# Kernel tuning notes

Measured on AMD Instinct MI355X. Metric: run time of the kernel, lower is better.

Reference implementation:

```python
import jax, jax.numpy as jnp
import numpy as np

B, S, D = 1, 2048, 4096
H, KVH, DH = 32, 8, 128          # nheads, kv heads, head dim (GQA expansion = 4)
HID = 11008                       # 256 * ceil(4096 * (8/3) / 256)
EPS = 1e-5
ROPE_BASE = 10000.0


def setup_inputs() -> dict:
    key = jax.random.key(0)
    ks = jax.random.split(key, 10)
    std = 0.02
    w = lambda k, shape: jax.random.normal(k, shape, dtype=jnp.float32) * std
    return {
        "x": jax.random.normal(ks[0], (B, S, D), dtype=jnp.float32),
        "position_ids": jnp.broadcast_to(jnp.arange(S, dtype=jnp.int32), (B, S)),
        "ln_w": jnp.ones((D,), dtype=jnp.float32),
        "ffln_w": jnp.ones((D,), dtype=jnp.float32),
        "wq": w(ks[1], (D, H * DH)),
        "wk": w(ks[2], (D, KVH * DH)),
        "wv": w(ks[3], (D, KVH * DH)),
        "wo": w(ks[4], (H * DH, D)),
        "wg": w(ks[5], (D, HID)),
        "w1": w(ks[6], (D, HID)),
        "w2": w(ks[7], (HID, D)),
    }


def rmsnorm(x, w, eps=EPS):
    # LayerNormParameterized(use_mean=False, use_high_precision_pow=True)
    xf = x.astype(jnp.float32)
    var = jnp.mean(xf * xf, axis=-1, keepdims=True)
    return (xf * jax.lax.rsqrt(var + eps)).astype(x.dtype) * w


def rope(x, pos):
    # interleaved (complex-pair) rotary embedding; x: [B,S,h,DH], pos: [B,S]
    dh = x.shape[-1]
    inv_freq = 1.0 / (ROPE_BASE ** (jnp.arange(0, dh, 2, dtype=jnp.float32) / dh))
    ang = pos.astype(jnp.float32)[:, :, None, None] * inv_freq  # [B,S,1,dh/2]
    cos, sin = jnp.cos(ang), jnp.sin(ang)
    x1, x2 = x[..., 0::2], x[..., 1::2]
    return jnp.stack([x1 * cos - x2 * sin, x1 * sin + x2 * cos], axis=-1).reshape(x.shape)


def block(x, position_ids, ln_w, ffln_w, wq, wk, wv, wo, wg, w1, w2):
    # --- attention sublayer ---
    a = rmsnorm(x, ln_w)
    q = (a @ wq).reshape(B, S, H, DH)
    k = (a @ wk).reshape(B, S, KVH, DH)
    v = (a @ wv).reshape(B, S, KVH, DH)
    q = rope(q, position_ids)
    k = rope(k, position_ids)
    # GQA expansion: kv head g serves query heads [g*exp, (g+1)*exp)
    exp = H // KVH
    k_e = jnp.repeat(k, exp, axis=2)  # [B,S,H,DH]
    v_e = jnp.repeat(v, exp, axis=2)
    scores = jnp.einsum("bqhd,bkhd->bhqk", q, k_e) / np.sqrt(DH).astype(np.float32)
    causal = jnp.tril(jnp.ones((S, S), dtype=bool))
    scores = jnp.where(causal, scores, jnp.finfo(scores.dtype).min)
    p = jax.nn.softmax(scores, axis=-1)
    attn = jnp.einsum("bhqk,bkhd->bqhd", p, v_e).reshape(B, S, H * DH)
    x = x + attn @ wo
    # --- SwiGLU FFN sublayer ---
    b = rmsnorm(x, ffln_w)
    ff = (jax.nn.silu(b @ wg) * (b @ w1)) @ w2
    return x + ff


def reference(x, position_ids, ln_w, ffln_w, wq, wk, wv, wo, wg, w1, w2):
    return block(x, position_ids, ln_w, ffln_w, wq, wk, wv, wo, wg, w1, w2)
```

## Files before the change

kernel.cpp:

```cpp
#include <hip/hip_runtime.h>
#include <hip/hip_bf16.h>

typedef __bf16 bf16_t;
typedef __bf16 bf16x4 __attribute__((ext_vector_type(4)));
typedef __bf16 bf16x8 __attribute__((ext_vector_type(8)));
typedef float f32x4 __attribute__((ext_vector_type(4)));

#define S_ 2048
#define D_ 4096
#define H_ 32
#define KVH_ 8
#define DH_ 128
#define HID_ 11008
#define QKV_N 6144
#define GU_N 22016

__device__ __forceinline__ void gl16(const bf16_t* g, bf16_t* l) {
  __builtin_amdgcn_global_load_lds(
      (const __attribute__((address_space(1))) unsigned int*)g,
      (__attribute__((address_space(3))) unsigned int*)l, 16, 0, 0);
}

#define VMW(N)                                          \
  asm volatile("s_waitcnt vmcnt(" #N ")" ::: "memory"); \
  __builtin_amdgcn_sched_barrier(0)

#define LGKM(N)                                           \
  asm volatile("s_waitcnt lgkmcnt(" #N ")" ::: "memory"); \
  __builtin_amdgcn_sched_barrier(0)

#define BAR()                          \
  asm volatile("" ::: "memory");       \
  __builtin_amdgcn_s_barrier();        \
  asm volatile("" ::: "memory")

__global__ __launch_bounds__(256) void rmsnorm_kernel(
    const float* __restrict__ x, const float* __restrict__ w,
    bf16_t* __restrict__ out) {
  int row = blockIdx.x;
  const float* xr = x + (size_t)row * D_;
  float ss = 0.f;
  #pragma unroll
  for (int it = 0; it < 4; ++it) {
    int i = threadIdx.x * 4 + it * 1024;
    float4 v = *(const float4*)(xr + i);
    ss += v.x * v.x + v.y * v.y + v.z * v.z + v.w * v.w;
  }
  #pragma unroll
  for (int off = 32; off; off >>= 1) ss += __shfl_xor(ss, off);
  __shared__ float s4[4];
  if ((threadIdx.x & 63) == 0) s4[threadIdx.x >> 6] = ss;
  __syncthreads();
  float tot = s4[0] + s4[1] + s4[2] + s4[3];
  float rinv = rsqrtf(tot / (float)D_ + 1e-5f);
  bf16_t* orow = out + (size_t)row * D_;
  #pragma unroll
  for (int it = 0; it < 4; ++it) {
    int i = threadIdx.x * 4 + it * 1024;
    float4 v = *(const float4*)(xr + i);
    orow[i + 0] = (bf16_t)(v.x * rinv * w[i + 0]);
    orow[i + 1] = (bf16_t)(v.y * rinv * w[i + 1]);
    orow[i + 2] = (bf16_t)(v.z * rinv * w[i + 2]);
    orow[i + 3] = (bf16_t)(v.w * rinv * w[i + 3]);
  }
}

__global__ __launch_bounds__(256) void combine_rms_kernel(
    const float* __restrict__ x, const float* __restrict__ p0,
    const float* __restrict__ p1, const float* __restrict__ w,
    float* __restrict__ x1, bf16_t* __restrict__ out) {
  int row = blockIdx.x;
  size_t base = (size_t)row * D_;
  float ss = 0.f;
  float4 vals[4];
  #pragma unroll
  for (int it = 0; it < 4; ++it) {
    int i = threadIdx.x * 4 + it * 1024;
    float4 a = *(const float4*)(x + base + i);
    float4 b = *(const float4*)(p0 + base + i);
    float4 c = *(const float4*)(p1 + base + i);
    float4 v;
    v.x = a.x + b.x + c.x; v.y = a.y + b.y + c.y;
    v.z = a.z + b.z + c.z; v.w = a.w + b.w + c.w;
    vals[it] = v;
    *(float4*)(x1 + base + i) = v;
    ss += v.x * v.x + v.y * v.y + v.z * v.z + v.w * v.w;
  }
  #pragma unroll
  for (int off = 32; off; off >>= 1) ss += __shfl_xor(ss, off);
  __shared__ float s4[4];
  if ((threadIdx.x & 63) == 0) s4[threadIdx.x >> 6] = ss;
  __syncthreads();
  float tot = s4[0] + s4[1] + s4[2] + s4[3];
  float rinv = rsqrtf(tot / (float)D_ + 1e-5f);
  #pragma unroll
  for (int it = 0; it < 4; ++it) {
    int i = threadIdx.x * 4 + it * 1024;
    float4 v = vals[it];
    out[base + i + 0] = (bf16_t)(v.x * rinv * w[i + 0]);
    out[base + i + 1] = (bf16_t)(v.y * rinv * w[i + 1]);
    out[base + i + 2] = (bf16_t)(v.z * rinv * w[i + 2]);
    out[base + i + 3] = (bf16_t)(v.w * rinv * w[i + 3]);
  }
}

__global__ __launch_bounds__(256) void combine_out_kernel(
    const float* __restrict__ x1, const float* __restrict__ p0,
    const float* __restrict__ p1, float* __restrict__ outp) {
  size_t i = ((size_t)blockIdx.x * 256 + threadIdx.x) * 4;
  float4 a = *(const float4*)(x1 + i);
  float4 b = *(const float4*)(p0 + i);
  float4 c = *(const float4*)(p1 + i);
  float4 v;
  v.x = a.x + b.x + c.x; v.y = a.y + b.y + c.y;
  v.z = a.z + b.z + c.z; v.w = a.w + b.w + c.w;
  *(float4*)(outp + i) = v;
}

__global__ __launch_bounds__(256) void wtrans_kernel(
    const float* __restrict__ W, bf16_t* __restrict__ WT, int K, int N) {
  __shared__ bf16_t t[32][258];
  int k0 = blockIdx.x * 32, n0 = blockIdx.y * 256;
  #pragma unroll
  for (int i = 0; i < 8; ++i) {
    int flat = i * 1024 + threadIdx.x * 4;
    int kk = flat >> 8, nn = flat & 255;
    float4 wv = *(const float4*)(W + (size_t)(k0 + kk) * N + n0 + nn);
    bf16_t* p = &t[kk][nn];
    p[0] = (bf16_t)wv.x; p[1] = (bf16_t)wv.y;
    p[2] = (bf16_t)wv.z; p[3] = (bf16_t)wv.w;
  }
  __syncthreads();
  int kc8 = (threadIdx.x & 3) * 8;
  #pragma unroll
  for (int i = 0; i < 4; ++i) {
    int nn = i * 64 + (threadIdx.x >> 2);
    bf16x8 vals;
    #pragma unroll
    for (int j = 0; j < 8; ++j) vals[j] = t[kc8 + j][nn];
    *(bf16x8*)(WT + (size_t)(n0 + nn) * K + k0 + kc8) = vals;
  }
}

__global__ __launch_bounds__(256) void vtrans_kernel(
    const bf16_t* __restrict__ qkv, bf16_t* __restrict__ vt) {
  __shared__ bf16_t t[64][72];
  int s0 = blockIdx.x * 64, d0 = blockIdx.y * 64;
  #pragma unroll
  for (int it = 0; it < 2; ++it) {
    int r = (threadIdx.x >> 3) + it * 32;
    int c = (threadIdx.x & 7) * 8;
    *(bf16x8*)&t[r][c] =
        *(const bf16x8*)(qkv + (size_t)(s0 + r) * QKV_N + 5120 + d0 + c);
  }
  __syncthreads();
  #pragma unroll
  for (int it = 0; it < 2; ++it) {
    int c = threadIdx.x & 63;
    int sb = (threadIdx.x >> 6) * 16 + it * 8;
    bf16x8 v;
    #pragma unroll
    for (int j = 0; j < 8; ++j) v[j] = t[sb + j][c];
    *(bf16x8*)(vt + (size_t)(d0 + c) * S_ + s0 + sb) = v;
  }
}

__global__ __launch_bounds__(256) void rope_table_kernel(
    const int* __restrict__ pos_ids, float* __restrict__ cos_t,
    float* __restrict__ sin_t) {
  int idx = blockIdx.x * 256 + threadIdx.x;
  int s = idx >> 6, i = idx & 63;
  float pos = (float)pos_ids[s];
  float inv_freq = exp2f(-(float)i * (13.287712379549449f / 64.0f));
  float ang = pos * inv_freq;
  cos_t[idx] = cosf(ang);
  sin_t[idx] = sinf(ang);
}

__global__ __launch_bounds__(256) void rope_kernel(
    bf16_t* __restrict__ buf, const float* __restrict__ cos_t,
    const float* __restrict__ sin_t, int nheads, int colbase, int total) {
  int idx = blockIdx.x * 256 + threadIdx.x;
  if (idx >= total) return;
  int i = idx & 63;
  int t2 = idx >> 6;
  int s = t2 / nheads, h = t2 % nheads;
  size_t base = (size_t)s * QKV_N + colbase + h * 128 + 2 * i;
  float x1 = (float)buf[base], x2 = (float)buf[base + 1];
  float c = cos_t[s * 64 + i], sn = sin_t[s * 64 + i];
  buf[base]     = (bf16_t)(x1 * c - x2 * sn);
  buf[base + 1] = (bf16_t)(x1 * sn + x2 * c);
}


#define READ_A(dst, BIx, KK, MH)                                           \
  _Pragma("unroll") for (int m = 0; m < 4; ++m)                            \
    dst[m] = *(const bf16x8*)&lds[BIx][0][wr][KK]                          \
        [((MH) * 64 + m * 16 + fr) * 32 + rc * 8];

#define READ_B(dst, BIx, KK)                                               \
  _Pragma("unroll") for (int n = 0; n < 4; ++n)                            \
    dst[n] = *(const bf16x8*)&lds[BIx][1][wcH][KK]                         \
        [(wcL * 64 + n * 16 + fr) * 32 + rc * 8];

#define MFMA16(aS, bS, MH)                                                 \
  __builtin_amdgcn_s_setprio(1);                                           \
  _Pragma("unroll") for (int m = 0; m < 4; ++m)                            \
    _Pragma("unroll") for (int n = 0; n < 4; ++n)                          \
      acc[(MH) * 4 + m][n] = __builtin_amdgcn_mfma_f32_16x16x32_bf16(      \
          aS[m], bS[n], acc[(MH) * 4 + m][n], 0, 0, 0);                    \
  __builtin_amdgcn_s_setprio(0);

#define DO_TILE(BI, T)                                                     \
  {                                                                        \
    const int Tp1 = (T) + 1 < NT, Tp2 = (T) + 2 < NT;                      \
    if (Tp1) {                                                             \
      stage(BI ^ 1, 0, 0, 1, (T) + 1); stage(BI ^ 1, 1, 0, 1, (T) + 1);    \
      stage(BI ^ 1, 0, 1, 1, (T) + 1); stage(BI ^ 1, 1, 1, 1, (T) + 1);    \
    }                                                                      \
    READ_A(aF, BI, 0, 0); READ_B(bF, BI, 0);                               \
    LGKM(0);                                                               \
    MFMA16(aF, bF, 0);                                                     \
    READ_A(aF, BI, 0, 1);                                                  \
    LGKM(0);                                                               \
    MFMA16(aF, bF, 1);                                                     \
    BAR();                     \
    if (Tp2) {                                                             \
      stage(BI, 0, 0, 0, (T) + 2); stage(BI, 1, 0, 0, (T) + 2);            \
      stage(BI, 0, 1, 0, (T) + 2); stage(BI, 1, 1, 0, (T) + 2);            \
    }                                                                      \
    READ_A(aF, BI, 1, 0); READ_B(bF, BI, 1);                               \
    LGKM(0);                                                               \
    MFMA16(aF, bF, 0);                                                     \
    READ_A(aF, BI, 1, 1);                                                  \
    LGKM(0);                                                               \
    MFMA16(aF, bF, 1);                                                     \
    if (Tp2) { VMW(4); } else if (Tp1) { VMW(0); }                         \
    BAR();        \
  }

template <int MODE, int SPLIT>
__global__ __launch_bounds__(512, 2) void gemm256_kernel(
    const bf16_t* __restrict__ A, int lda, const bf16_t* __restrict__ BT,
    int ldb, void* __restrict__ Cout, int ldc, int K) {
  __shared__ __align__(16) bf16_t lds[2][2][2][2][128 * 32];

  const int tid = threadIdx.x;
  const int lane = tid & 63;
  const int wid = tid >> 6;
  const int wr = wid >> 2;
  const int wc = wid & 3;
  const int wcH = wc >> 1, wcL = wc & 1;
  const int g = lane >> 4, fr = lane & 15;
  const int rc = (g + ((fr >> 1) & 3)) & 3;

  const int nwg = gridDim.x;
  const int orig = blockIdx.x;
  int wg = (orig & 7) * (nwg >> 3) + (orig >> 3);
  int kz = 0;
  if constexpr (SPLIT) {
    const int half = nwg >> 1;
    kz = wg >= half;
    wg -= kz * half;
  }
  const int bx = wg & 7;
  const int by = wg >> 3;
  const size_t row0 = (size_t)bx * 256, col0 = (size_t)by * 256;

  const int srow = tid >> 2;
  const int schunk = ((tid & 3) - ((tid >> 3) & 3)) & 3;

  const size_t lda2 = (size_t)lda * 2, ldb2 = (size_t)ldb * 2;
  const size_t kzoff = (size_t)kz * K * 2;
  const char* aB0 =
      (const char*)A + (row0 + srow) * lda2 + schunk * 16 + kzoff;
  const char* aB1 = aB0 + (size_t)128 * lda2;
  const char* bB0 =
      (const char*)BT + (col0 + srow) * ldb2 + schunk * 16 + kzoff;
  const char* bB1 = bB0 + (size_t)128 * ldb2;

  auto stage = [&](int bi, int ab, int h, int kk, int kt) {
    const char* base = ab ? (h ? bB1 : bB0) : (h ? aB1 : aB0);
    gl16((const bf16_t*)(base + (size_t)kt * 128 + kk * 64),
         &lds[bi][ab][h][kk][tid * 8]);
  };

  f32x4 acc[8][4] = {};
  bf16x8 aF[4], bF[4];
  const int NT = K / 64;

  stage(0, 0, 0, 0, 0); stage(0, 1, 0, 0, 0);
  stage(0, 0, 1, 0, 0); stage(0, 1, 1, 0, 0);
  stage(0, 0, 0, 1, 0); stage(0, 1, 0, 1, 0);
  stage(0, 0, 1, 1, 0); stage(0, 1, 1, 1, 0);
  stage(1, 0, 0, 0, 1); stage(1, 1, 0, 0, 1);
  stage(1, 0, 1, 0, 1); stage(1, 1, 1, 0, 1);
  VMW(4);
  BAR();

  for (int T = 0; T < NT; T += 2) {
    DO_TILE(0, T);
    DO_TILE(1, T + 1);
  }

  float* fOut = (float*)Cout + (size_t)kz * 2048 * ldc;
  #pragma unroll
  for (int mf = 0; mf < 8; ++mf)
    #pragma unroll
    for (int n = 0; n < 4; ++n)
      #pragma unroll
      for (int r = 0; r < 4; ++r) {
        size_t row = row0 + wr * 128 + mf * 16 + g * 4 + r;
        size_t col = col0 + wc * 64 + n * 16 + fr;
        float val = acc[mf][n][r];
        if constexpr (MODE == 0) {
          ((bf16_t*)Cout)[row * ldc + col] = (bf16_t)val;
        } else {
          fOut[row * ldc + col] = val;
        }
      }
}

__global__ __launch_bounds__(256, 2) void attn_kernel(
    const bf16_t* __restrict__ qkv, const bf16_t* __restrict__ vt,
    bf16_t* __restrict__ o) {
  int h = blockIdx.y;
  int qb = (S_ / 64 - 1) - blockIdx.x;
  int kvh = h >> 2;
  int tid = threadIdx.x;
  int wid = tid >> 6, lane = tid & 63;
  int g = lane >> 4, fr = lane & 15;

  __shared__ __align__(16) bf16_t kfl[2][8192];
  __shared__ __align__(16) bf16_t vfl[2][8192];
  __shared__ __align__(16) bf16_t p_lds[4][16][72];

  const int fr_s = (tid >> 2) & 15, g_s = tid & 3;
  const int kcw = (tid >> 6) & 3;
  const int kc2w = (tid >> 6) & 1;
  const int nhi = tid >> 7;
  const bf16_t* kSrc = qkv + (size_t)fr_s * QKV_N + 4096 + kvh * 128 +
                       (kcw * 4 + g_s) * 8;
  const bf16_t* vSrc = vt + ((size_t)kvh * 128 + nhi * 16 + fr_s) * S_ +
                       (kc2w * 4 + g_s) * 8;

  auto stage = [&](int bi, int t) {
    size_t kv0 = (size_t)t * 64;
    #pragma unroll
    for (int i = 0; i < 4; ++i)
      gl16(kSrc + (kv0 + i * 16) * QKV_N, &kfl[bi][(i * 256 + tid) * 8]);
    #pragma unroll
    for (int i = 0; i < 4; ++i)
      gl16(vSrc + (size_t)i * 32 * S_ + kv0, &vfl[bi][(i * 256 + tid) * 8]);
  };

  int q0w = qb * 64 + wid * 16;
  bf16x8 q_frag[4];
  const bf16_t* qptr = qkv + (size_t)(q0w + fr) * QKV_N + h * 128;
  #pragma unroll
  for (int kc = 0; kc < 4; ++kc)
    q_frag[kc] = *(const bf16x8*)(qptr + kc * 32 + g * 8);
  VMW(0);

  stage(0, 0);

  f32x4 o_frag[8] = {};
  float m_run[4], l_run[4];
  #pragma unroll
  for (int r = 0; r < 4; ++r) { m_run[r] = -1e30f; l_run[r] = 0.f; }

  const float sc = 0.08838834764831845f * 1.4426950408889634f;

  for (int t = 0; t <= qb; ++t) {
    int cur = t & 1;
    int kv0 = t * 64;
    if (t < qb) {
      stage(cur ^ 1, t + 1);
      VMW(8);
    } else {
      VMW(0);
    }
    BAR();

    f32x4 sfr[4];
    #pragma unroll
    for (int nf = 0; nf < 4; ++nf) {
      f32x4 acc = {};
      #pragma unroll
      for (int kc = 0; kc < 4; ++kc) {
        bf16x8 kf =
            *(const bf16x8*)&kfl[cur][(nf * 256 + kc * 64 + fr * 4 + g) * 8];
        acc = __builtin_amdgcn_mfma_f32_16x16x32_bf16(q_frag[kc], kf, acc, 0, 0, 0);
      }
      sfr[nf] = acc;
    }

    bool diag = (t == qb);
    float mtile[4];
    #pragma unroll
    for (int r = 0; r < 4; ++r) mtile[r] = -1e30f;
    #pragma unroll
    for (int nf = 0; nf < 4; ++nf)
      #pragma unroll
      for (int r = 0; r < 4; ++r) {
        if (diag) {
          int kvg = kv0 + nf * 16 + fr;
          int qg = q0w + 4 * g + r;
          if (kvg > qg) sfr[nf][r] = -1e30f;
        }
        mtile[r] = fmaxf(mtile[r], sfr[nf][r]);
      }
    #pragma unroll
    for (int r = 0; r < 4; ++r) {
      float mv = mtile[r];
      mv = fmaxf(mv, __shfl_xor(mv, 1));
      mv = fmaxf(mv, __shfl_xor(mv, 2));
      mv = fmaxf(mv, __shfl_xor(mv, 4));
      mv = fmaxf(mv, __shfl_xor(mv, 8));
      mtile[r] = mv;
    }
    float alpha[4];
    #pragma unroll
    for (int r = 0; r < 4; ++r) {
      float m_new = fmaxf(m_run[r], mtile[r]);
      alpha[r] = exp2f((m_run[r] - m_new) * sc);
      m_run[r] = m_new;
    }
    float lsum[4] = {0.f, 0.f, 0.f, 0.f};
    #pragma unroll
    for (int nf = 0; nf < 4; ++nf)
      #pragma unroll
      for (int r = 0; r < 4; ++r) {
        float p = exp2f((sfr[nf][r] - m_run[r]) * sc);
        sfr[nf][r] = p;
        lsum[r] += p;
      }
    #pragma unroll
    for (int r = 0; r < 4; ++r) {
      float lv = lsum[r];
      lv += __shfl_xor(lv, 1);
      lv += __shfl_xor(lv, 2);
      lv += __shfl_xor(lv, 4);
      lv += __shfl_xor(lv, 8);
      l_run[r] = l_run[r] * alpha[r] + lv;
    }
    #pragma unroll
    for (int nfo = 0; nfo < 8; ++nfo)
      #pragma unroll
      for (int r = 0; r < 4; ++r) o_frag[nfo][r] *= alpha[r];

    #pragma unroll
    for (int nf = 0; nf < 4; ++nf)
      #pragma unroll
      for (int r = 0; r < 4; ++r)
        p_lds[wid][4 * g + r][nf * 16 + fr] = (bf16_t)sfr[nf][r];

    #pragma unroll
    for (int kc2 = 0; kc2 < 2; ++kc2) {
      bf16x8 pf = *(const bf16x8*)&p_lds[wid][fr][kc2 * 32 + g * 8];
      #pragma unroll
      for (int nfo = 0; nfo < 8; ++nfo) {
        bf16x8 vf =
            *(const bf16x8*)&vfl[cur][(nfo * 128 + kc2 * 64 + fr * 4 + g) * 8];
        o_frag[nfo] = __builtin_amdgcn_mfma_f32_16x16x32_bf16(pf, vf, o_frag[nfo], 0, 0, 0);
      }
    }
    BAR();
  }

  #pragma unroll
  for (int nfo = 0; nfo < 8; ++nfo)
    #pragma unroll
    for (int r = 0; r < 4; ++r) {
      int qg = q0w + 4 * g + r;
      float val = o_frag[nfo][r] / l_run[r];
      o[(size_t)qg * (H_ * DH_) + h * DH_ + nfo * 16 + fr] = (bf16_t)val;
    }
}

__global__ __launch_bounds__(256) void silu_mul_kernel(bf16_t* __restrict__ gu) {
  size_t idx = (size_t)blockIdx.x * 256 + threadIdx.x;
  int r = (int)(idx / (HID_ / 8));
  int c8 = (int)(idx % (HID_ / 8));
  bf16_t* p = gu + (size_t)r * GU_N + c8 * 8;
  bf16x8 g8 = *(const bf16x8*)p;
  bf16x8 u8 = *(const bf16x8*)(p + HID_);
  bf16x8 h8;
  #pragma unroll
  for (int j = 0; j < 8; ++j) {
    float gv = (float)g8[j];
    float uv = (float)u8[j];
    h8[j] = (bf16_t)(gv / (1.f + __expf(-gv)) * uv);
  }
  *(bf16x8*)p = h8;
}

extern "C" void kernel_launch(void* const* d_in, const int* in_sizes, int n_in,
                              void* d_out, int out_size, void* d_ws,
                              size_t ws_size, hipStream_t stream) {
  const float* x = (const float*)d_in[0];
  const int* pos = (const int*)d_in[1];
  const float* ln_w = (const float*)d_in[2];
  const float* ffln_w = (const float*)d_in[3];
  const float* wq = (const float*)d_in[4];
  const float* wk = (const float*)d_in[5];
  const float* wv = (const float*)d_in[6];
  const float* wo = (const float*)d_in[7];
  const float* wg = (const float*)d_in[8];
  const float* w1 = (const float*)d_in[9];
  const float* w2 = (const float*)d_in[10];

  char* ws = (char*)d_ws;
  size_t off = 0;
  auto alloc = [&](size_t bytes) {
    size_t o = off;
    off = (off + bytes + 255) & ~(size_t)255;
    return o;
  };
  bf16_t* Wbuf = (bf16_t*)(ws + alloc((size_t)GU_N * D_ * 2));
  bf16_t* nbuf = (bf16_t*)(ws + alloc((size_t)S_ * D_ * 2));
  bf16_t* qkv  = (bf16_t*)(ws + alloc((size_t)S_ * QKV_N * 2));
  float*  x1   = (float*)(ws + alloc((size_t)S_ * D_ * 4));
  bf16_t* gu   = (bf16_t*)(ws + alloc((size_t)S_ * GU_N * 2));
  bf16_t* vtb  = (bf16_t*)(ws + alloc((size_t)KVH_ * DH_ * S_ * 2));
  float*  cos_t = (float*)(ws + alloc((size_t)S_ * 64 * 4));
  float*  sin_t = (float*)(ws + alloc((size_t)S_ * 64 * 4));
  float* part = (float*)((char*)Wbuf + ((size_t)96 << 20));

  rmsnorm_kernel<<<S_, 256, 0, stream>>>(x, ln_w, nbuf);
  wtrans_kernel<<<dim3(D_ / 32, D_ / 256), 256, 0, stream>>>(wq, Wbuf, D_, D_);
  wtrans_kernel<<<dim3(D_ / 32, 1024 / 256), 256, 0, stream>>>(
      wk, Wbuf + (size_t)4096 * D_, D_, 1024);
  wtrans_kernel<<<dim3(D_ / 32, 1024 / 256), 256, 0, stream>>>(
      wv, Wbuf + (size_t)5120 * D_, D_, 1024);
  rope_table_kernel<<<(S_ * 64) / 256, 256, 0, stream>>>(pos, cos_t, sin_t);
  gemm256_kernel<0, 0><<<dim3((S_ / 256) * (QKV_N / 256)), 512, 0, stream>>>(
      nbuf, D_, Wbuf, D_, qkv, QKV_N, D_);
  rope_kernel<<<(S_ * H_ * 64) / 256, 256, 0, stream>>>(
      qkv, cos_t, sin_t, H_, 0, S_ * H_ * 64);
  rope_kernel<<<(S_ * KVH_ * 64) / 256, 256, 0, stream>>>(
      qkv, cos_t, sin_t, KVH_, 4096, S_ * KVH_ * 64);
  vtrans_kernel<<<dim3(S_ / 64, (KVH_ * DH_) / 64), 256, 0, stream>>>(qkv, vtb);
  attn_kernel<<<dim3(S_ / 64, H_), 256, 0, stream>>>(qkv, vtb, nbuf);
  wtrans_kernel<<<dim3(D_ / 32, D_ / 256), 256, 0, stream>>>(wo, Wbuf, D_, D_);
  gemm256_kernel<2, 1><<<dim3((S_ / 256) * (D_ / 256) * 2), 512, 0, stream>>>(
      nbuf, D_, Wbuf, D_, part, D_, 2048);
  combine_rms_kernel<<<S_, 256, 0, stream>>>(
      x, part, part + (size_t)S_ * D_, ffln_w, x1, nbuf);
  wtrans_kernel<<<dim3(D_ / 32, HID_ / 256), 256, 0, stream>>>(wg, Wbuf, D_, HID_);
  wtrans_kernel<<<dim3(D_ / 32, HID_ / 256), 256, 0, stream>>>(
      w1, Wbuf + (size_t)HID_ * D_, D_, HID_);
  gemm256_kernel<0, 0><<<dim3((S_ / 256) * (GU_N / 256)), 512, 0, stream>>>(
      nbuf, D_, Wbuf, D_, gu, GU_N, D_);
  silu_mul_kernel<<<(S_ * HID_ / 8) / 256, 256, 0, stream>>>(gu);
  wtrans_kernel<<<dim3(HID_ / 32, D_ / 256), 256, 0, stream>>>(w2, Wbuf, HID_, D_);
  gemm256_kernel<2, 1><<<dim3((S_ / 256) * (D_ / 256) * 2), 512, 0, stream>>>(
      gu, GU_N, Wbuf, HID_, part, D_, 5504);
  combine_out_kernel<<<(S_ * D_ / 4) / 256, 256, 0, stream>>>(
      x1, part, part + (size_t)S_ * D_, (float*)d_out);
}
```

Before: 1.204 ms.

## Use 1024-thread GEMM blocks with 64x64 per-wave tiles and simpler pipeline

The 256x256 GEMM goes from 8 waves to 16 waves per block. Each wave now owns a 64x64 output subtile instead of 128x64, which halves the accumulator registers. The deeper split-k-half prefetch schedule is replaced by a single-stage double buffer that waits for all loads (vmcnt 0) every K-tile. The aim is more waves in flight and lower register pressure, at the cost of more LDS reads per MFMA and less overlap between loads and compute. Launch bounds of (1024,4) may force heavy register limits or spills.

```diff
diff --git a/kernel.cpp b/kernel.cpp
--- a/kernel.cpp
+++ b/kernel.cpp
@@ -193,64 +193,35 @@
 }
 
 
-#define READ_A(dst, BIx, KK, MH)                                           \
+#define READ_A(dst, BIx, KK)                                               \
   _Pragma("unroll") for (int m = 0; m < 4; ++m)                            \
-    dst[m] = *(const bf16x8*)&lds[BIx][0][wr][KK]                          \
-        [((MH) * 64 + m * 16 + fr) * 32 + rc * 8];
+    dst[m] = *(const bf16x8*)&lds[BIx][0][KK]                              \
+        [(wr * 64 + m * 16 + fr) * 32 + rc * 8];
 
 #define READ_B(dst, BIx, KK)                                               \
   _Pragma("unroll") for (int n = 0; n < 4; ++n)                            \
-    dst[n] = *(const bf16x8*)&lds[BIx][1][wcH][KK]                         \
-        [(wcL * 64 + n * 16 + fr) * 32 + rc * 8];
-
-#define MFMA16(aS, bS, MH)                                                 \
+    dst[n] = *(const bf16x8*)&lds[BIx][1][KK]                              \
+        [(wc * 64 + n * 16 + fr) * 32 + rc * 8];
+
+#define MFMA16(aS, bS)                                                     \
   __builtin_amdgcn_s_setprio(1);                                           \
   _Pragma("unroll") for (int m = 0; m < 4; ++m)                            \
     _Pragma("unroll") for (int n = 0; n < 4; ++n)                          \
-      acc[(MH) * 4 + m][n] = __builtin_amdgcn_mfma_f32_16x16x32_bf16(      \
-          aS[m], bS[n], acc[(MH) * 4 + m][n], 0, 0, 0);                    \
+      acc[m][n] = __builtin_amdgcn_mfma_f32_16x16x32_bf16(                 \
+          aS[m], bS[n], acc[m][n], 0, 0, 0);                               \
   __builtin_amdgcn_s_setprio(0);
 
-#define DO_TILE(BI, T)                                                     \
-  {                                                                        \
-    const int Tp1 = (T) + 1 < NT, Tp2 = (T) + 2 < NT;                      \
-    if (Tp1) {                                                             \
-      stage(BI ^ 1, 0, 0, 1, (T) + 1); stage(BI ^ 1, 1, 0, 1, (T) + 1);    \
-      stage(BI ^ 1, 0, 1, 1, (T) + 1); stage(BI ^ 1, 1, 1, 1, (T) + 1);    \
-    }                                                                      \
-    READ_A(aF, BI, 0, 0); READ_B(bF, BI, 0);                               \
-    LGKM(0);                                                               \
-    MFMA16(aF, bF, 0);                                                     \
-    READ_A(aF, BI, 0, 1);                                                  \
-    LGKM(0);                                                               \
-    MFMA16(aF, bF, 1);                                                     \
-    BAR();                     \
-    if (Tp2) {                                                             \
-      stage(BI, 0, 0, 0, (T) + 2); stage(BI, 1, 0, 0, (T) + 2);            \
-      stage(BI, 0, 1, 0, (T) + 2); stage(BI, 1, 1, 0, (T) + 2);            \
-    }                                                                      \
-    READ_A(aF, BI, 1, 0); READ_B(bF, BI, 1);                               \
-    LGKM(0);                                                               \
-    MFMA16(aF, bF, 0);                                                     \
-    READ_A(aF, BI, 1, 1);                                                  \
-    LGKM(0);                                                               \
-    MFMA16(aF, bF, 1);                                                     \
-    if (Tp2) { VMW(4); } else if (Tp1) { VMW(0); }                         \
-    BAR();        \
-  }
-
 template <int MODE, int SPLIT>
-__global__ __launch_bounds__(512, 2) void gemm256_kernel(
+__global__ __launch_bounds__(1024, 4) void gemm256_kernel(
     const bf16_t* __restrict__ A, int lda, const bf16_t* __restrict__ BT,
     int ldb, void* __restrict__ Cout, int ldc, int K) {
-  __shared__ __align__(16) bf16_t lds[2][2][2][2][128 * 32];
+  __shared__ __align__(16) bf16_t lds[2][2][2][256 * 32];
 
   const int tid = threadIdx.x;
   const int lane = tid & 63;
   const int wid = tid >> 6;
   const int wr = wid >> 2;
   const int wc = wid & 3;
-  const int wcH = wc >> 1, wcL = wc & 1;
   const int g = lane >> 4, fr = lane & 15;
   const int rc = (g + ((fr >> 1) & 3)) & 3;
 
@@ -272,47 +243,53 @@
 
   const size_t lda2 = (size_t)lda * 2, ldb2 = (size_t)ldb * 2;
   const size_t kzoff = (size_t)kz * K * 2;
-  const char* aB0 =
+  const char* aB =
       (const char*)A + (row0 + srow) * lda2 + schunk * 16 + kzoff;
-  const char* aB1 = aB0 + (size_t)128 * lda2;
-  const char* bB0 =
+  const char* bB =
       (const char*)BT + (col0 + srow) * ldb2 + schunk * 16 + kzoff;
-  const char* bB1 = bB0 + (size_t)128 * ldb2;
-
-  auto stage = [&](int bi, int ab, int h, int kk, int kt) {
-    const char* base = ab ? (h ? bB1 : bB0) : (h ? aB1 : aB0);
+
+  auto stage = [&](int bi, int ab, int kk, int kt) {
+    const char* base = ab ? bB : aB;
     gl16((const bf16_t*)(base + (size_t)kt * 128 + kk * 64),
-         &lds[bi][ab][h][kk][tid * 8]);
+         &lds[bi][ab][kk][tid * 8]);
   };
 
-  f32x4 acc[8][4] = {};
+  f32x4 acc[4][4] = {};
   bf16x8 aF[4], bF[4];
   const int NT = K / 64;
 
-  stage(0, 0, 0, 0, 0); stage(0, 1, 0, 0, 0);
-  stage(0, 0, 1, 0, 0); stage(0, 1, 1, 0, 0);
-  stage(0, 0, 0, 1, 0); stage(0, 1, 0, 1, 0);
-  stage(0, 0, 1, 1, 0); stage(0, 1, 1, 1, 0);
-  stage(1, 0, 0, 0, 1); stage(1, 1, 0, 0, 1);
-  stage(1, 0, 1, 0, 1); stage(1, 1, 1, 0, 1);
-  VMW(4);
+  stage(0, 0, 0, 0); stage(0, 1, 0, 0);
+  stage(0, 0, 1, 0); stage(0, 1, 1, 0);
+  VMW(0);
   BAR();
 
-  for (int T = 0; T < NT; T += 2) {
-    DO_TILE(0, T);
-    DO_TILE(1, T + 1);
+  for (int T = 0; T < NT; ++T) {
+    const int BI = T & 1;
+    const int Tp1 = T + 1 < NT;
+    if (Tp1) {
+      stage(BI ^ 1, 0, 0, T + 1); stage(BI ^ 1, 1, 0, T + 1);
+      stage(BI ^ 1, 0, 1, T + 1); stage(BI ^ 1, 1, 1, T + 1);
+    }
+    READ_A(aF, BI, 0); READ_B(bF, BI, 0);
+    LGKM(0);
+    MFMA16(aF, bF);
+    READ_A(aF, BI, 1); READ_B(bF, BI, 1);
+    LGKM(0);
+    MFMA16(aF, bF);
+    VMW(0);
+    BAR();
   }
 
   float* fOut = (float*)Cout + (size_t)kz * 2048 * ldc;
   #pragma unroll
-  for (int mf = 0; mf < 8; ++mf)
+  for (int m = 0; m < 4; ++m)
     #pragma unroll
     for (int n = 0; n < 4; ++n)
       #pragma unroll
       for (int r = 0; r < 4; ++r) {
-        size_t row = row0 + wr * 128 + mf * 16 + g * 4 + r;
+        size_t row = row0 + wr * 64 + m * 16 + g * 4 + r;
         size_t col = col0 + wc * 64 + n * 16 + fr;
-        float val = acc[mf][n][r];
+        float val = acc[m][n][r];
         if constexpr (MODE == 0) {
           ((bf16_t*)Cout)[row * ldc + col] = (bf16_t)val;
         } else {
@@ -534,7 +511,7 @@
   wtrans_kernel<<<dim3(D_ / 32, 1024 / 256), 256, 0, stream>>>(
       wv, Wbuf + (size_t)5120 * D_, D_, 1024);
   rope_table_kernel<<<(S_ * 64) / 256, 256, 0, stream>>>(pos, cos_t, sin_t);
-  gemm256_kernel<0, 0><<<dim3((S_ / 256) * (QKV_N / 256)), 512, 0, stream>>>(
+  gemm256_kernel<0, 0><<<dim3((S_ / 256) * (QKV_N / 256)), 1024, 0, stream>>>(
       nbuf, D_, Wbuf, D_, qkv, QKV_N, D_);
   rope_kernel<<<(S_ * H_ * 64) / 256, 256, 0, stream>>>(
       qkv, cos_t, sin_t, H_, 0, S_ * H_ * 64);
@@ -543,18 +520,18 @@
   vtrans_kernel<<<dim3(S_ / 64, (KVH_ * DH_) / 64), 256, 0, stream>>>(qkv, vtb);
   attn_kernel<<<dim3(S_ / 64, H_), 256, 0, stream>>>(qkv, vtb, nbuf);
   wtrans_kernel<<<dim3(D_ / 32, D_ / 256), 256, 0, stream>>>(wo, Wbuf, D_, D_);
-  gemm256_kernel<2, 1><<<dim3((S_ / 256) * (D_ / 256) * 2), 512, 0, stream>>>(
+  gemm256_kernel<2, 1><<<dim3((S_ / 256) * (D_ / 256) * 2), 1024, 0, stream>>>(
       nbuf, D_, Wbuf, D_, part, D_, 2048);
   combine_rms_kernel<<<S_, 256, 0, stream>>>(
       x, part, part + (size_t)S_ * D_, ffln_w, x1, nbuf);
   wtrans_kernel<<<dim3(D_ / 32, HID_ / 256), 256, 0, stream>>>(wg, Wbuf, D_, HID_);
   wtrans_kernel<<<dim3(D_ / 32, HID_ / 256), 256, 0, stream>>>(
       w1, Wbuf + (size_t)HID_ * D_, D_, HID_);
-  gemm256_kernel<0, 0><<<dim3((S_ / 256) * (GU_N / 256)), 512, 0, stream>>>(
+  gemm256_kernel<0, 0><<<dim3((S_ / 256) * (GU_N / 256)), 1024, 0, stream>>>(
       nbuf, D_, Wbuf, D_, gu, GU_N, D_);
   silu_mul_kernel<<<(S_ * HID_ / 8) / 256, 256, 0, stream>>>(gu);
   wtrans_kernel<<<dim3(HID_ / 32, D_ / 256), 256, 0, stream>>>(w2, Wbuf, HID_, D_);
-  gemm256_kernel<2, 1><<<dim3((S_ / 256) * (D_ / 256) * 2), 512, 0, stream>>>(
+  gemm256_kernel<2, 1><<<dim3((S_ / 256) * (D_ / 256) * 2), 1024, 0, stream>>>(
       gu, GU_N, Wbuf, HID_, part, D_, 5504);
   combine_out_kernel<<<(S_ * D_ / 4) / 256, 256, 0, stream>>>(
       x1, part, part + (size_t)S_ * D_, (float*)d_out);
```

Measured after the change: 1.194 ms. No clear change (-0.8%).
